# Performance work log

Hardware: AMD Instinct MI355X
Metric: run time of the kernel (lower is better)

Reference implementation:

```python
import jax, jax.numpy as jnp
import numpy as np

H, I, E, TOPK = 2048, 1408, 8, 2
B, S = 2, 2048


def setup_inputs() -> dict:
    key = jax.random.key(0)
    k1, k2, k3, k4, k5 = jax.random.split(key, 5)
    x = jax.random.normal(k1, (B, S, H), dtype=jnp.float32)
    expert_indices = jax.random.randint(k2, (B, S, TOPK), 0, E, dtype=jnp.int64)
    expert_weights = jax.random.uniform(k3, (B, S, TOPK), dtype=jnp.float32)
    # params: w13 = concat([gate, up], dim=1) -> [E, 2I, H]; down_proj [E, H, I]
    w13 = jax.random.normal(k4, (E, 2 * I, H), dtype=jnp.float32) * 0.02
    down_proj = jax.random.normal(k5, (E, H, I), dtype=jnp.float32) * 0.02
    return {"x": x, "expert_indices": expert_indices, "expert_weights": expert_weights,
            "w13": w13, "down_proj": down_proj}


def _moe(x, expert_indices, expert_weights, w13, down_proj):
    b, s, h = x.shape
    T = b * s
    x_flat = x.reshape(T, h)
    idx = expert_indices.reshape(T, -1)            # [T, top_k]
    wts = expert_weights.reshape(T, -1)            # [T, top_k]
    # dense combine weights: routing[t, e] = sum of weights of slots routed to e
    # (matches original scatter/index_add combine, including duplicate experts)
    routing = jnp.zeros((T, w13.shape[0]), x.dtype).at[
        jnp.arange(T)[:, None], idx].add(wts)      # [T, E]
    # per-expert SwiGLU MLP computed densely, zeroed out by routing weights
    gu = jnp.einsum('th,eih->tei', x_flat, w13)    # [T, E, 2I]
    g, u = jnp.split(gu, 2, axis=-1)
    hact = jax.nn.silu(g) * u                      # [T, E, I]
    y = jnp.einsum('tei,ehi->teh', hact, down_proj)  # [T, E, H]
    out = jnp.einsum('te,teh->th', routing, y)     # [T, H]
    return out.reshape(b, s, h)


def reference(x, expert_indices, expert_weights, w13, down_proj):
    return _moe(x, expert_indices, expert_weights, w13, down_proj)
```

## Files before the change

### kernel.cpp

```cpp
#include <hip/hip_runtime.h>
#include <hip/hip_bf16.h>


typedef __bf16 bf16;
typedef bf16 bf16x8 __attribute__((ext_vector_type(8)));
typedef float f32x4 __attribute__((ext_vector_type(4)));

constexpr int Hdim = 2048;
constexpr int Idim = 1408;
constexpr int NE = 8;
constexpr int TOPK = 2;
constexpr int NT = 4096;
constexpr int NPAIR = 8192;
constexpr int BK = 64;

#define GLOAD16(G, L) __builtin_amdgcn_global_load_lds(                    \
    (const __attribute__((address_space(1))) void*)(G),                    \
    (__attribute__((address_space(3))) void*)(L), 16, 0, 0)


__global__ void k_cvt(const float* __restrict__ src, bf16* __restrict__ dst, int n8) {
    int i = blockIdx.x * 256 + threadIdx.x;
    if (i >= n8) return;
    f32x4 a = *reinterpret_cast<const f32x4*>(src + (size_t)i * 8);
    f32x4 b = *reinterpret_cast<const f32x4*>(src + (size_t)i * 8 + 4);
    bf16x8 v;
#pragma unroll
    for (int j = 0; j < 4; j++) { v[j] = (bf16)a[j]; v[4 + j] = (bf16)b[j]; }
    *reinterpret_cast<bf16x8*>(dst + (size_t)i * 8) = v;
}


__global__ void k_bin1(const int* __restrict__ eidx, int* __restrict__ chunkhist) {
    __shared__ int h[NE];
    int t = threadIdx.x;
    if (t < NE) h[t] = 0;
    __syncthreads();
    int p = blockIdx.x * 256 + t;
    atomicAdd(&h[eidx[p]], 1);
    __syncthreads();
    if (t < NE) chunkhist[blockIdx.x * NE + t] = h[t];
}

__global__ void k_bin2(int* __restrict__ meta, const int* __restrict__ chunkhist,
                       int* __restrict__ chunkbase) {
    if (threadIdx.x == 0) {
        int counts[NE];
        for (int e = 0; e < NE; e++) counts[e] = 0;
        for (int b = 0; b < 32; b++)
            for (int e = 0; e < NE; e++) {
                chunkbase[b * NE + e] = counts[e];
                counts[e] += chunkhist[b * NE + e];
            }
        int acc = 0;
        for (int e = 0; e < NE; e++) {
            meta[e] = counts[e];
            meta[8 + e] = acc;
            acc += counts[e];
        }
    }
}

__global__ void k_bin3(const int* __restrict__ eidx, const float* __restrict__ wts,
                       const int* __restrict__ meta, const int* __restrict__ chunkbase,
                       int* __restrict__ token_id, float* __restrict__ weightv) {
    __shared__ int earr[256];
    int t = threadIdx.x;
    int p = blockIdx.x * 256 + t;
    int e = eidx[p];
    earr[t] = e;
    __syncthreads();
    int rank = 0;
    for (int q = 0; q < t; q++) rank += (earr[q] == e) ? 1 : 0;
    int pos = meta[8 + e] + chunkbase[blockIdx.x * NE + e] + rank;
    token_id[pos] = p / TOPK;
    weightv[pos] = wts[p];
}


__global__ __launch_bounds__(256, 2) void k_gemm1(
    const bf16* __restrict__ xb, const bf16* __restrict__ w13b,
    const int* __restrict__ meta, bf16* __restrict__ hact) {
    const int flat = blockIdx.x;
    const int work = (flat & 7) * 704 + (flat >> 3);
    const int mslot = work & 63;
    const int grp = work >> 6;
    const int e = grp / 11;
    const int ytile = grp - e * 11;

    const int n_e = meta[e];
    const int m0 = mslot * 128;
    if (m0 >= n_e) return;
    const int base = meta[8 + e];
    const int* toks = (const int*)(meta + 64) + base;
    const bf16* wg = w13b + (size_t)e * (2 * Idim) * Hdim + (size_t)(ytile * 128) * Hdim;
    const bf16* wu = wg + (size_t)Idim * Hdim;

    __shared__ bf16 As[128 * 64];
    __shared__ bf16 Bg[128 * 64];
    __shared__ bf16 Bu[128 * 64];

    const int tid = threadIdx.x;
    const int lane = tid & 63;
    const int wid = tid >> 6;
    const int wr = wid >> 1, wc = wid & 1;
    const int l16 = lane & 15, lq = lane >> 4;

    const bf16* gA[4];
    const bf16* gG[4];
    const bf16* gU[4];
    int lo[4];
#pragma unroll
    for (int r = 0; r < 4; r++) {
        int sid = r * 256 + tid;
        int row = sid >> 3, seg = sid & 7;
        int ss = seg ^ (row & 7);
        lo[r] = (r * 256 + (tid & ~63)) * 16;
        int rr = m0 + row;
        if (rr >= n_e) rr = n_e - 1;
        gA[r] = xb + (size_t)toks[rr] * Hdim + ss * 8;
        gG[r] = wg + (size_t)row * Hdim + ss * 8;
        gU[r] = wu + (size_t)row * Hdim + ss * 8;
    }

    f32x4 accg[4][4], accu[4][4];
#pragma unroll
    for (int m = 0; m < 4; m++)
#pragma unroll
        for (int n = 0; n < 4; n++) {
            accg[m][n] = f32x4{0.f, 0.f, 0.f, 0.f};
            accu[m][n] = f32x4{0.f, 0.f, 0.f, 0.f};
        }

    for (int k0 = 0; k0 < Hdim; k0 += BK) {
        __syncthreads();
#pragma unroll
        for (int r = 0; r < 4; r++) {
            GLOAD16(gA[r] + k0, (char*)As + lo[r]);
            GLOAD16(gG[r] + k0, (char*)Bg + lo[r]);
            GLOAD16(gU[r] + k0, (char*)Bu + lo[r]);
        }
        __syncthreads();
#pragma unroll
        for (int kk = 0; kk < 2; ++kk) {
            bf16x8 af[4], bgf[4], buf_[4];
#pragma unroll
            for (int m = 0; m < 4; m++) {
                int row = wr * 64 + m * 16 + l16;
                int s = (kk * 4 + lq) ^ (row & 7);
                af[m] = *reinterpret_cast<const bf16x8*>(&As[row * 64 + s * 8]);
            }
#pragma unroll
            for (int n = 0; n < 4; n++) {
                int row = wc * 64 + n * 16 + l16;
                int s = (kk * 4 + lq) ^ (row & 7);
                bgf[n] = *reinterpret_cast<const bf16x8*>(&Bg[row * 64 + s * 8]);
                buf_[n] = *reinterpret_cast<const bf16x8*>(&Bu[row * 64 + s * 8]);
            }
#pragma unroll
            for (int m = 0; m < 4; m++)
#pragma unroll
                for (int n = 0; n < 4; n++) {
                    accg[m][n] = __builtin_amdgcn_mfma_f32_16x16x32_bf16(af[m], bgf[n], accg[m][n], 0, 0, 0);
                    accu[m][n] = __builtin_amdgcn_mfma_f32_16x16x32_bf16(af[m], buf_[n], accu[m][n], 0, 0, 0);
                }
        }
    }

    const int colbase = ytile * 128 + wc * 64;
#pragma unroll
    for (int m = 0; m < 4; m++) {
        int lr0 = m0 + wr * 64 + m * 16 + lq * 4;
#pragma unroll
        for (int j = 0; j < 4; j++) {
            int lr = lr0 + j;
            if (lr < n_e) {
                size_t rowoff = (size_t)(base + lr) * Idim;
#pragma unroll
                for (int n = 0; n < 4; n++) {
                    float g = accg[m][n][j], u = accu[m][n][j];
                    float v = (g / (1.f + __expf(-g))) * u;
                    hact[rowoff + colbase + n * 16 + l16] = (bf16)v;
                }
            }
        }
    }
}


__global__ __launch_bounds__(256, 2) void k_gemm2(
    const bf16* __restrict__ hact, const bf16* __restrict__ dpb,
    const int* __restrict__ meta, const float* __restrict__ weightv,
    float* __restrict__ out) {
    const int flat = blockIdx.x;
    const int work = (flat & 7) * 1024 + (flat >> 3);
    const int mslot = work & 63;
    const int grp = work >> 6;
    const int e = grp >> 4;
    const int ytile = grp & 15;

    const int n_e = meta[e];
    const int m0 = mslot * 128;
    if (m0 >= n_e) return;
    const int base = meta[8 + e];
    const int* toks = (const int*)(meta + 64) + base;
    const bf16* wb = dpb + (size_t)e * Hdim * Idim + (size_t)(ytile * 128) * Idim;

    __shared__ bf16 As[128 * 64];
    __shared__ bf16 Bs[128 * 64];

    const int tid = threadIdx.x;
    const int lane = tid & 63;
    const int wid = tid >> 6;
    const int wr = wid >> 1, wc = wid & 1;
    const int l16 = lane & 15, lq = lane >> 4;

    const bf16* gA[4];
    const bf16* gB[4];
    int lo[4];
#pragma unroll
    for (int r = 0; r < 4; r++) {
        int sid = r * 256 + tid;
        int row = sid >> 3, seg = sid & 7;
        int ss = seg ^ (row & 7);
        lo[r] = (r * 256 + (tid & ~63)) * 16;
        int rr = m0 + row;
        if (rr >= n_e) rr = n_e - 1;
        gA[r] = hact + (size_t)(base + rr) * Idim + ss * 8;
        gB[r] = wb + (size_t)row * Idim + ss * 8;
    }

    f32x4 acc[4][4];
#pragma unroll
    for (int m = 0; m < 4; m++)
#pragma unroll
        for (int n = 0; n < 4; n++) acc[m][n] = f32x4{0.f, 0.f, 0.f, 0.f};

    for (int k0 = 0; k0 < Idim; k0 += BK) {
        __syncthreads();
#pragma unroll
        for (int r = 0; r < 4; r++) {
            GLOAD16(gA[r] + k0, (char*)As + lo[r]);
            GLOAD16(gB[r] + k0, (char*)Bs + lo[r]);
        }
        __syncthreads();
#pragma unroll
        for (int kk = 0; kk < 2; ++kk) {
            bf16x8 af[4], bf_[4];
#pragma unroll
            for (int m = 0; m < 4; m++) {
                int row = wr * 64 + m * 16 + l16;
                int s = (kk * 4 + lq) ^ (row & 7);
                af[m] = *reinterpret_cast<const bf16x8*>(&As[row * 64 + s * 8]);
            }
#pragma unroll
            for (int n = 0; n < 4; n++) {
                int row = wc * 64 + n * 16 + l16;
                int s = (kk * 4 + lq) ^ (row & 7);
                bf_[n] = *reinterpret_cast<const bf16x8*>(&Bs[row * 64 + s * 8]);
            }
#pragma unroll
            for (int m = 0; m < 4; m++)
#pragma unroll
                for (int n = 0; n < 4; n++)
                    acc[m][n] = __builtin_amdgcn_mfma_f32_16x16x32_bf16(af[m], bf_[n], acc[m][n], 0, 0, 0);
        }
    }

    const int colbase = ytile * 128 + wc * 64;
#pragma unroll
    for (int m = 0; m < 4; m++) {
        int lr0 = m0 + wr * 64 + m * 16 + lq * 4;
#pragma unroll
        for (int j = 0; j < 4; j++) {
            int lr = lr0 + j;
            if (lr < n_e) {
                int tok = toks[lr];
                float w = weightv[base + lr];
#pragma unroll
                for (int n = 0; n < 4; n++) {
                    float v = acc[m][n][j] * w;
                    unsafeAtomicAdd(&out[(size_t)tok * Hdim + colbase + n * 16 + l16], v);
                }
            }
        }
    }
}


extern "C" void kernel_launch(void* const* d_in, const int* in_sizes, int n_in,
                              void* d_out, int out_size, void* d_ws, size_t ws_size,
                              hipStream_t stream) {
    const float* x = (const float*)d_in[0];
    const int* eidx = (const int*)d_in[1];
    const float* ewts = (const float*)d_in[2];
    const float* w13 = (const float*)d_in[3];
    const float* dproj = (const float*)d_in[4];
    float* out = (float*)d_out;

    char* ws = (char*)d_ws;
    int* meta = (int*)ws;
    int* token_id = meta + 64;
    float* weightv = (float*)(meta + 64 + NPAIR);
    int* chunkhist = meta + 64 + 2 * NPAIR;
    int* chunkbase = chunkhist + 256;
    bf16* xb = (bf16*)(ws + 67840);
    bf16* w13b = xb + (size_t)NT * Hdim;
    bf16* dpb = w13b + (size_t)NE * 2 * Idim * Hdim;
    bf16* hact = dpb + (size_t)NE * Hdim * Idim;

    hipMemsetAsync(d_out, 0, (size_t)out_size * sizeof(float), stream);

    const int nx8 = NT * Hdim / 8;
    const int nw8 = NE * 2 * Idim * Hdim / 8;
    const int nd8 = NE * Hdim * Idim / 8;
    k_cvt<<<(nx8 + 255) / 256, 256, 0, stream>>>(x, xb, nx8);
    k_cvt<<<(nw8 + 255) / 256, 256, 0, stream>>>(w13, w13b, nw8);
    k_cvt<<<(nd8 + 255) / 256, 256, 0, stream>>>(dproj, dpb, nd8);

    k_bin1<<<32, 256, 0, stream>>>(eidx, chunkhist);
    k_bin2<<<1, 64, 0, stream>>>(meta, chunkhist, chunkbase);
    k_bin3<<<32, 256, 0, stream>>>(eidx, ewts, meta, chunkbase, token_id, weightv);

    k_gemm1<<<5632, 256, 0, stream>>>(xb, w13b, meta, hact);
    k_gemm2<<<8192, 256, 0, stream>>>(hact, dpb, meta, weightv, out);
}
```

Before: 354.5 us.

## Double-buffer LDS with BK=32 stages in both MoE GEMM kernels

```diff
diff --git a/kernel.cpp b/kernel.cpp
--- a/kernel.cpp
+++ b/kernel.cpp
@@ -12,7 +12,6 @@
 constexpr int TOPK = 2;
 constexpr int NT = 4096;
 constexpr int NPAIR = 8192;
-constexpr int BK = 64;
 
 #define GLOAD16(G, L) __builtin_amdgcn_global_load_lds(                    \
     (const __attribute__((address_space(1))) void*)(G),                    \
@@ -78,7 +77,7 @@
 }
 
 
-__global__ __launch_bounds__(256, 2) void k_gemm1(
+__global__ __launch_bounds__(256, 3) void k_gemm1(
     const bf16* __restrict__ xb, const bf16* __restrict__ w13b,
     const int* __restrict__ meta, bf16* __restrict__ hact) {
     const int flat = blockIdx.x;
@@ -96,9 +95,8 @@
     const bf16* wg = w13b + (size_t)e * (2 * Idim) * Hdim + (size_t)(ytile * 128) * Hdim;
     const bf16* wu = wg + (size_t)Idim * Hdim;
 
-    __shared__ bf16 As[128 * 64];
-    __shared__ bf16 Bg[128 * 64];
-    __shared__ bf16 Bu[128 * 64];
+    __shared__ bf16 buf0[12288];
+    __shared__ bf16 buf1[12288];
 
     const int tid = threadIdx.x;
     const int lane = tid & 63;
@@ -106,21 +104,24 @@
     const int wr = wid >> 1, wc = wid & 1;
     const int l16 = lane & 15, lq = lane >> 4;
 
-    const bf16* gA[4];
-    const bf16* gG[4];
-    const bf16* gU[4];
-    int lo[4];
-#pragma unroll
-    for (int r = 0; r < 4; r++) {
-        int sid = r * 256 + tid;
-        int row = sid >> 3, seg = sid & 7;
-        int ss = seg ^ (row & 7);
-        lo[r] = (r * 256 + (tid & ~63)) * 16;
-        int rr = m0 + row;
-        if (rr >= n_e) rr = n_e - 1;
-        gA[r] = xb + (size_t)toks[rr] * Hdim + ss * 8;
-        gG[r] = wg + (size_t)row * Hdim + ss * 8;
-        gU[r] = wu + (size_t)row * Hdim + ss * 8;
+    const bf16* gp[6];
+    int lo[6];
+#pragma unroll
+    for (int r = 0; r < 6; r++) {
+        int rr = r & 1;
+        int s = rr * 256 + tid;
+        int row = s >> 2, seg = s & 3;
+        int ss = seg ^ ((row >> 1) & 3);
+        lo[r] = (r >> 1) * 8192 + (rr * 256 + (tid & ~63)) * 16;
+        if (r < 2) {
+            int rm = m0 + row;
+            if (rm >= n_e) rm = n_e - 1;
+            gp[r] = xb + (size_t)toks[rm] * Hdim + ss * 8;
+        } else if (r < 4) {
+            gp[r] = wg + (size_t)row * Hdim + ss * 8;
+        } else {
+            gp[r] = wu + (size_t)row * Hdim + ss * 8;
+        }
     }
 
     f32x4 accg[4][4], accu[4][4];
@@ -132,39 +133,49 @@
             accu[m][n] = f32x4{0.f, 0.f, 0.f, 0.f};
         }
 
-    for (int k0 = 0; k0 < Hdim; k0 += BK) {
+#define STAGE1(BUF, K0)                                                     \
+    {                                                                       \
+        _Pragma("unroll")                                                   \
+        for (int r = 0; r < 6; r++) GLOAD16(gp[r] + (K0), (char*)(BUF) + lo[r]); \
+    }
+
+#define COMP1(BUF)                                                          \
+    {                                                                       \
+        const bf16* As_ = (BUF);                                            \
+        const bf16* Bg_ = (BUF) + 4096;                                     \
+        const bf16* Bu_ = (BUF) + 8192;                                     \
+        bf16x8 af[4], bgf[4], buf_[4];                                      \
+        _Pragma("unroll")                                                   \
+        for (int m = 0; m < 4; m++) {                                       \
+            int row = wr * 64 + m * 16 + l16;                               \
+            int s = lq ^ ((row >> 1) & 3);                                  \
+            af[m] = *reinterpret_cast<const bf16x8*>(&As_[row * 32 + s * 8]); \
+        }                                                                   \
+        _Pragma("unroll")                                                   \
+        for (int n = 0; n < 4; n++) {                                       \
+            int row = wc * 64 + n * 16 + l16;                               \
+            int s = lq ^ ((row >> 1) & 3);                                  \
+            bgf[n] = *reinterpret_cast<const bf16x8*>(&Bg_[row * 32 + s * 8]); \
+            buf_[n] = *reinterpret_cast<const bf16x8*>(&Bu_[row * 32 + s * 8]); \
+        }                                                                   \
+        _Pragma("unroll")                                                   \
+        for (int m = 0; m < 4; m++)                                         \
+            _Pragma("unroll")                                               \
+            for (int n = 0; n < 4; n++) {                                   \
+                accg[m][n] = __builtin_amdgcn_mfma_f32_16x16x32_bf16(af[m], bgf[n], accg[m][n], 0, 0, 0); \
+                accu[m][n] = __builtin_amdgcn_mfma_f32_16x16x32_bf16(af[m], buf_[n], accu[m][n], 0, 0, 0); \
+            }                                                               \
+    }
+
+    STAGE1(buf0, 0);
+    __syncthreads();
+    for (int k = 0; k < Hdim; k += 64) {
+        STAGE1(buf1, k + 32);
+        COMP1(buf0);
         __syncthreads();
-#pragma unroll
-        for (int r = 0; r < 4; r++) {
-            GLOAD16(gA[r] + k0, (char*)As + lo[r]);
-            GLOAD16(gG[r] + k0, (char*)Bg + lo[r]);
-            GLOAD16(gU[r] + k0, (char*)Bu + lo[r]);
-        }
+        if (k + 64 < Hdim) STAGE1(buf0, k + 64);
+        COMP1(buf1);
         __syncthreads();
-#pragma unroll
-        for (int kk = 0; kk < 2; ++kk) {
-            bf16x8 af[4], bgf[4], buf_[4];
-#pragma unroll
-            for (int m = 0; m < 4; m++) {
-                int row = wr * 64 + m * 16 + l16;
-                int s = (kk * 4 + lq) ^ (row & 7);
-                af[m] = *reinterpret_cast<const bf16x8*>(&As[row * 64 + s * 8]);
-            }
-#pragma unroll
-            for (int n = 0; n < 4; n++) {
-                int row = wc * 64 + n * 16 + l16;
-                int s = (kk * 4 + lq) ^ (row & 7);
-                bgf[n] = *reinterpret_cast<const bf16x8*>(&Bg[row * 64 + s * 8]);
-                buf_[n] = *reinterpret_cast<const bf16x8*>(&Bu[row * 64 + s * 8]);
-            }
-#pragma unroll
-            for (int m = 0; m < 4; m++)
-#pragma unroll
-                for (int n = 0; n < 4; n++) {
-                    accg[m][n] = __builtin_amdgcn_mfma_f32_16x16x32_bf16(af[m], bgf[n], accg[m][n], 0, 0, 0);
-                    accu[m][n] = __builtin_amdgcn_mfma_f32_16x16x32_bf16(af[m], buf_[n], accu[m][n], 0, 0, 0);
-                }
-        }
     }
 
     const int colbase = ytile * 128 + wc * 64;
@@ -185,10 +196,12 @@
             }
         }
     }
-}
-
-
-__global__ __launch_bounds__(256, 2) void k_gemm2(
+#undef STAGE1
+#undef COMP1
+}
+
+
+__global__ __launch_bounds__(256, 4) void k_gemm2(
     const bf16* __restrict__ hact, const bf16* __restrict__ dpb,
     const int* __restrict__ meta, const float* __restrict__ weightv,
     float* __restrict__ out) {
@@ -206,8 +219,8 @@
     const int* toks = (const int*)(meta + 64) + base;
     const bf16* wb = dpb + (size_t)e * Hdim * Idim + (size_t)(ytile * 128) * Idim;
 
-    __shared__ bf16 As[128 * 64];
-    __shared__ bf16 Bs[128 * 64];
+    __shared__ bf16 c0[8192];
+    __shared__ bf16 c1[8192];
 
     const int tid = threadIdx.x;
     const int lane = tid & 63;
@@ -215,19 +228,22 @@
     const int wr = wid >> 1, wc = wid & 1;
     const int l16 = lane & 15, lq = lane >> 4;
 
-    const bf16* gA[4];
-    const bf16* gB[4];
+    const bf16* gp[4];
     int lo[4];
 #pragma unroll
     for (int r = 0; r < 4; r++) {
-        int sid = r * 256 + tid;
-        int row = sid >> 3, seg = sid & 7;
-        int ss = seg ^ (row & 7);
-        lo[r] = (r * 256 + (tid & ~63)) * 16;
-        int rr = m0 + row;
-        if (rr >= n_e) rr = n_e - 1;
-        gA[r] = hact + (size_t)(base + rr) * Idim + ss * 8;
-        gB[r] = wb + (size_t)row * Idim + ss * 8;
+        int rr = r & 1;
+        int s = rr * 256 + tid;
+        int row = s >> 2, seg = s & 3;
+        int ss = seg ^ ((row >> 1) & 3);
+        lo[r] = (r >> 1) * 8192 + (rr * 256 + (tid & ~63)) * 16;
+        if (r < 2) {
+            int rm = m0 + row;
+            if (rm >= n_e) rm = n_e - 1;
+            gp[r] = hact + (size_t)(base + rm) * Idim + ss * 8;
+        } else {
+            gp[r] = wb + (size_t)row * Idim + ss * 8;
+        }
     }
 
     f32x4 acc[4][4];
@@ -236,35 +252,45 @@
 #pragma unroll
         for (int n = 0; n < 4; n++) acc[m][n] = f32x4{0.f, 0.f, 0.f, 0.f};
 
-    for (int k0 = 0; k0 < Idim; k0 += BK) {
+#define STAGE2(BUF, K0)                                                     \
+    {                                                                       \
+        _Pragma("unroll")                                                   \
+        for (int r = 0; r < 4; r++) GLOAD16(gp[r] + (K0), (char*)(BUF) + lo[r]); \
+    }
+
+#define COMP2(BUF)                                                          \
+    {                                                                       \
+        const bf16* As_ = (BUF);                                            \
+        const bf16* Bs_ = (BUF) + 4096;                                     \
+        bf16x8 af[4], bf_[4];                                               \
+        _Pragma("unroll")                                                   \
+        for (int m = 0; m < 4; m++) {                                       \
+            int row = wr * 64 + m * 16 + l16;                               \
+            int s = lq ^ ((row >> 1) & 3);                                  \
+            af[m] = *reinterpret_cast<const bf16x8*>(&As_[row * 32 + s * 8]); \
+        }                                                                   \
+        _Pragma("unroll")                                                   \
+        for (int n = 0; n < 4; n++) {                                       \
+            int row = wc * 64 + n * 16 + l16;                               \
+            int s = lq ^ ((row >> 1) & 3);                                  \
+            bf_[n] = *reinterpret_cast<const bf16x8*>(&Bs_[row * 32 + s * 8]); \
+        }                                                                   \
+        _Pragma("unroll")                                                   \
+        for (int m = 0; m < 4; m++)                                         \
+            _Pragma("unroll")                                               \
+            for (int n = 0; n < 4; n++)                                     \
+                acc[m][n] = __builtin_amdgcn_mfma_f32_16x16x32_bf16(af[m], bf_[n], acc[m][n], 0, 0, 0); \
+    }
+
+    STAGE2(c0, 0);
+    __syncthreads();
+    for (int k = 0; k < Idim; k += 64) {
+        STAGE2(c1, k + 32);
+        COMP2(c0);
         __syncthreads();
-#pragma unroll
-        for (int r = 0; r < 4; r++) {
-            GLOAD16(gA[r] + k0, (char*)As + lo[r]);
-            GLOAD16(gB[r] + k0, (char*)Bs + lo[r]);
-        }
+        if (k + 64 < Idim) STAGE2(c0, k + 64);
+        COMP2(c1);
         __syncthreads();
-#pragma unroll
-        for (int kk = 0; kk < 2; ++kk) {
-            bf16x8 af[4], bf_[4];
-#pragma unroll
-            for (int m = 0; m < 4; m++) {
-                int row = wr * 64 + m * 16 + l16;
-                int s = (kk * 4 + lq) ^ (row & 7);
-                af[m] = *reinterpret_cast<const bf16x8*>(&As[row * 64 + s * 8]);
-            }
-#pragma unroll
-            for (int n = 0; n < 4; n++) {
-                int row = wc * 64 + n * 16 + l16;
-                int s = (kk * 4 + lq) ^ (row & 7);
-                bf_[n] = *reinterpret_cast<const bf16x8*>(&Bs[row * 64 + s * 8]);
-            }
-#pragma unroll
-            for (int m = 0; m < 4; m++)
-#pragma unroll
-                for (int n = 0; n < 4; n++)
-                    acc[m][n] = __builtin_amdgcn_mfma_f32_16x16x32_bf16(af[m], bf_[n], acc[m][n], 0, 0, 0);
-        }
     }
 
     const int colbase = ytile * 128 + wc * 64;
@@ -285,6 +311,8 @@
             }
         }
     }
+#undef STAGE2
+#undef COMP2
 }
 
 
```

Result: slower. 802.4 us (+126.3%).

## Enlarge M tile to 256 rows in both grouped MoE GEMMs

Applied to the files above, without the earlier changes.

```diff
diff --git a/kernel.cpp b/kernel.cpp
--- a/kernel.cpp
+++ b/kernel.cpp
@@ -78,27 +78,137 @@
 }
 
 
-__global__ __launch_bounds__(256, 2) void k_gemm1(
+__global__ __launch_bounds__(512, 2) void k_gemm1(
     const bf16* __restrict__ xb, const bf16* __restrict__ w13b,
     const int* __restrict__ meta, bf16* __restrict__ hact) {
     const int flat = blockIdx.x;
-    const int work = (flat & 7) * 704 + (flat >> 3);
-    const int mslot = work & 63;
-    const int grp = work >> 6;
+    const int work = (flat & 7) * 352 + (flat >> 3);
+    const int mslot = work & 31;
+    const int grp = work >> 5;
     const int e = grp / 11;
     const int ytile = grp - e * 11;
 
     const int n_e = meta[e];
-    const int m0 = mslot * 128;
+    const int m0 = mslot * 256;
     if (m0 >= n_e) return;
     const int base = meta[8 + e];
     const int* toks = (const int*)(meta + 64) + base;
     const bf16* wg = w13b + (size_t)e * (2 * Idim) * Hdim + (size_t)(ytile * 128) * Hdim;
     const bf16* wu = wg + (size_t)Idim * Hdim;
 
-    __shared__ bf16 As[128 * 64];
-    __shared__ bf16 Bg[128 * 64];
-    __shared__ bf16 Bu[128 * 64];
+    __shared__ bf16 smem[32768];
+
+    const int tid = threadIdx.x;
+    const int lane = tid & 63;
+    const int wid = tid >> 6;
+    const int wr = wid >> 2, wc = wid & 3;
+    const int l16 = lane & 15, lq = lane >> 4;
+
+    const bf16* gp[8];
+    int lo[8];
+#pragma unroll
+    for (int r = 0; r < 8; r++) {
+        int q = (r < 4) ? r : ((r - 4) & 1);
+        int sid = q * 512 + tid;
+        int row = sid >> 3, seg = sid & 7;
+        int ss = seg ^ (row & 7);
+        if (r < 4) {
+            lo[r] = (r * 512 + (tid & ~63)) * 16;
+            int rm = m0 + row;
+            if (rm >= n_e) rm = n_e - 1;
+            gp[r] = xb + (size_t)toks[rm] * Hdim + ss * 8;
+        } else if (r < 6) {
+            lo[r] = 32768 + ((r - 4) * 512 + (tid & ~63)) * 16;
+            gp[r] = wg + (size_t)row * Hdim + ss * 8;
+        } else {
+            lo[r] = 49152 + ((r - 6) * 512 + (tid & ~63)) * 16;
+            gp[r] = wu + (size_t)row * Hdim + ss * 8;
+        }
+    }
+
+    f32x4 accg[8][2], accu[8][2];
+#pragma unroll
+    for (int m = 0; m < 8; m++)
+#pragma unroll
+        for (int n = 0; n < 2; n++) {
+            accg[m][n] = f32x4{0.f, 0.f, 0.f, 0.f};
+            accu[m][n] = f32x4{0.f, 0.f, 0.f, 0.f};
+        }
+
+    for (int k0 = 0; k0 < Hdim; k0 += BK) {
+        __syncthreads();
+#pragma unroll
+        for (int r = 0; r < 8; r++) GLOAD16(gp[r] + k0, (char*)smem + lo[r]);
+        __syncthreads();
+        const bf16* As = smem;
+        const bf16* Bg = smem + 16384;
+        const bf16* Bu = smem + 24576;
+#pragma unroll
+        for (int kk = 0; kk < 2; ++kk) {
+            bf16x8 af[8], bgf[2], buf_[2];
+#pragma unroll
+            for (int m = 0; m < 8; m++) {
+                int row = wr * 128 + m * 16 + l16;
+                int s = (kk * 4 + lq) ^ (row & 7);
+                af[m] = *reinterpret_cast<const bf16x8*>(&As[row * 64 + s * 8]);
+            }
+#pragma unroll
+            for (int n = 0; n < 2; n++) {
+                int row = wc * 32 + n * 16 + l16;
+                int s = (kk * 4 + lq) ^ (row & 7);
+                bgf[n] = *reinterpret_cast<const bf16x8*>(&Bg[row * 64 + s * 8]);
+                buf_[n] = *reinterpret_cast<const bf16x8*>(&Bu[row * 64 + s * 8]);
+            }
+#pragma unroll
+            for (int m = 0; m < 8; m++)
+#pragma unroll
+                for (int n = 0; n < 2; n++) {
+                    accg[m][n] = __builtin_amdgcn_mfma_f32_16x16x32_bf16(af[m], bgf[n], accg[m][n], 0, 0, 0);
+                    accu[m][n] = __builtin_amdgcn_mfma_f32_16x16x32_bf16(af[m], buf_[n], accu[m][n], 0, 0, 0);
+                }
+        }
+    }
+
+    const int colbase = ytile * 128 + wc * 32;
+#pragma unroll
+    for (int m = 0; m < 8; m++) {
+        int lr0 = m0 + wr * 128 + m * 16 + lq * 4;
+#pragma unroll
+        for (int j = 0; j < 4; j++) {
+            int lr = lr0 + j;
+            if (lr < n_e) {
+                size_t rowoff = (size_t)(base + lr) * Idim;
+#pragma unroll
+                for (int n = 0; n < 2; n++) {
+                    float g = accg[m][n][j], u = accu[m][n][j];
+                    float v = (g / (1.f + __expf(-g))) * u;
+                    hact[rowoff + colbase + n * 16 + l16] = (bf16)v;
+                }
+            }
+        }
+    }
+}
+
+
+__global__ __launch_bounds__(256, 3) void k_gemm2(
+    const bf16* __restrict__ hact, const bf16* __restrict__ dpb,
+    const int* __restrict__ meta, const float* __restrict__ weightv,
+    float* __restrict__ out) {
+    const int flat = blockIdx.x;
+    const int work = (flat & 7) * 512 + (flat >> 3);
+    const int mslot = work & 31;
+    const int grp = work >> 5;
+    const int e = grp >> 4;
+    const int ytile = grp & 15;
+
+    const int n_e = meta[e];
+    const int m0 = mslot * 256;
+    if (m0 >= n_e) return;
+    const int base = meta[8 + e];
+    const int* toks = (const int*)(meta + 64) + base;
+    const bf16* wb = dpb + (size_t)e * Hdim * Idim + (size_t)(ytile * 128) * Idim;
+
+    __shared__ bf16 smem[24576];
 
     const int tid = threadIdx.x;
     const int lane = tid & 63;
@@ -106,150 +216,44 @@
     const int wr = wid >> 1, wc = wid & 1;
     const int l16 = lane & 15, lq = lane >> 4;
 
-    const bf16* gA[4];
-    const bf16* gG[4];
-    const bf16* gU[4];
-    int lo[4];
-#pragma unroll
-    for (int r = 0; r < 4; r++) {
-        int sid = r * 256 + tid;
+    const bf16* gp[12];
+    int lo[12];
+#pragma unroll
+    for (int r = 0; r < 12; r++) {
+        int q = (r < 8) ? r : (r - 8);
+        int sid = q * 256 + tid;
         int row = sid >> 3, seg = sid & 7;
         int ss = seg ^ (row & 7);
-        lo[r] = (r * 256 + (tid & ~63)) * 16;
-        int rr = m0 + row;
-        if (rr >= n_e) rr = n_e - 1;
-        gA[r] = xb + (size_t)toks[rr] * Hdim + ss * 8;
-        gG[r] = wg + (size_t)row * Hdim + ss * 8;
-        gU[r] = wu + (size_t)row * Hdim + ss * 8;
-    }
-
-    f32x4 accg[4][4], accu[4][4];
-#pragma unroll
-    for (int m = 0; m < 4; m++)
-#pragma unroll
-        for (int n = 0; n < 4; n++) {
-            accg[m][n] = f32x4{0.f, 0.f, 0.f, 0.f};
-            accu[m][n] = f32x4{0.f, 0.f, 0.f, 0.f};
-        }
-
-    for (int k0 = 0; k0 < Hdim; k0 += BK) {
-        __syncthreads();
-#pragma unroll
-        for (int r = 0; r < 4; r++) {
-            GLOAD16(gA[r] + k0, (char*)As + lo[r]);
-            GLOAD16(gG[r] + k0, (char*)Bg + lo[r]);
-            GLOAD16(gU[r] + k0, (char*)Bu + lo[r]);
-        }
-        __syncthreads();
-#pragma unroll
-        for (int kk = 0; kk < 2; ++kk) {
-            bf16x8 af[4], bgf[4], buf_[4];
-#pragma unroll
-            for (int m = 0; m < 4; m++) {
-                int row = wr * 64 + m * 16 + l16;
-                int s = (kk * 4 + lq) ^ (row & 7);
-                af[m] = *reinterpret_cast<const bf16x8*>(&As[row * 64 + s * 8]);
-            }
-#pragma unroll
-            for (int n = 0; n < 4; n++) {
-                int row = wc * 64 + n * 16 + l16;
-                int s = (kk * 4 + lq) ^ (row & 7);
-                bgf[n] = *reinterpret_cast<const bf16x8*>(&Bg[row * 64 + s * 8]);
-                buf_[n] = *reinterpret_cast<const bf16x8*>(&Bu[row * 64 + s * 8]);
-            }
-#pragma unroll
-            for (int m = 0; m < 4; m++)
-#pragma unroll
-                for (int n = 0; n < 4; n++) {
-                    accg[m][n] = __builtin_amdgcn_mfma_f32_16x16x32_bf16(af[m], bgf[n], accg[m][n], 0, 0, 0);
-                    accu[m][n] = __builtin_amdgcn_mfma_f32_16x16x32_bf16(af[m], buf_[n], accu[m][n], 0, 0, 0);
-                }
-        }
-    }
-
-    const int colbase = ytile * 128 + wc * 64;
-#pragma unroll
-    for (int m = 0; m < 4; m++) {
-        int lr0 = m0 + wr * 64 + m * 16 + lq * 4;
-#pragma unroll
-        for (int j = 0; j < 4; j++) {
-            int lr = lr0 + j;
-            if (lr < n_e) {
-                size_t rowoff = (size_t)(base + lr) * Idim;
-#pragma unroll
-                for (int n = 0; n < 4; n++) {
-                    float g = accg[m][n][j], u = accu[m][n][j];
-                    float v = (g / (1.f + __expf(-g))) * u;
-                    hact[rowoff + colbase + n * 16 + l16] = (bf16)v;
-                }
-            }
-        }
-    }
-}
-
-
-__global__ __launch_bounds__(256, 2) void k_gemm2(
-    const bf16* __restrict__ hact, const bf16* __restrict__ dpb,
-    const int* __restrict__ meta, const float* __restrict__ weightv,
-    float* __restrict__ out) {
-    const int flat = blockIdx.x;
-    const int work = (flat & 7) * 1024 + (flat >> 3);
-    const int mslot = work & 63;
-    const int grp = work >> 6;
-    const int e = grp >> 4;
-    const int ytile = grp & 15;
-
-    const int n_e = meta[e];
-    const int m0 = mslot * 128;
-    if (m0 >= n_e) return;
-    const int base = meta[8 + e];
-    const int* toks = (const int*)(meta + 64) + base;
-    const bf16* wb = dpb + (size_t)e * Hdim * Idim + (size_t)(ytile * 128) * Idim;
-
-    __shared__ bf16 As[128 * 64];
-    __shared__ bf16 Bs[128 * 64];
-
-    const int tid = threadIdx.x;
-    const int lane = tid & 63;
-    const int wid = tid >> 6;
-    const int wr = wid >> 1, wc = wid & 1;
-    const int l16 = lane & 15, lq = lane >> 4;
-
-    const bf16* gA[4];
-    const bf16* gB[4];
-    int lo[4];
-#pragma unroll
-    for (int r = 0; r < 4; r++) {
-        int sid = r * 256 + tid;
-        int row = sid >> 3, seg = sid & 7;
-        int ss = seg ^ (row & 7);
-        lo[r] = (r * 256 + (tid & ~63)) * 16;
-        int rr = m0 + row;
-        if (rr >= n_e) rr = n_e - 1;
-        gA[r] = hact + (size_t)(base + rr) * Idim + ss * 8;
-        gB[r] = wb + (size_t)row * Idim + ss * 8;
-    }
-
-    f32x4 acc[4][4];
-#pragma unroll
-    for (int m = 0; m < 4; m++)
+        if (r < 8) {
+            lo[r] = (r * 256 + (tid & ~63)) * 16;
+            int rm = m0 + row;
+            if (rm >= n_e) rm = n_e - 1;
+            gp[r] = hact + (size_t)(base + rm) * Idim + ss * 8;
+        } else {
+            lo[r] = 32768 + ((r - 8) * 256 + (tid & ~63)) * 16;
+            gp[r] = wb + (size_t)row * Idim + ss * 8;
+        }
+    }
+
+    f32x4 acc[8][4];
+#pragma unroll
+    for (int m = 0; m < 8; m++)
 #pragma unroll
         for (int n = 0; n < 4; n++) acc[m][n] = f32x4{0.f, 0.f, 0.f, 0.f};
 
     for (int k0 = 0; k0 < Idim; k0 += BK) {
         __syncthreads();
 #pragma unroll
-        for (int r = 0; r < 4; r++) {
-            GLOAD16(gA[r] + k0, (char*)As + lo[r]);
-            GLOAD16(gB[r] + k0, (char*)Bs + lo[r]);
-        }
+        for (int r = 0; r < 12; r++) GLOAD16(gp[r] + k0, (char*)smem + lo[r]);
         __syncthreads();
+        const bf16* As = smem;
+        const bf16* Bs = smem + 16384;
 #pragma unroll
         for (int kk = 0; kk < 2; ++kk) {
-            bf16x8 af[4], bf_[4];
-#pragma unroll
-            for (int m = 0; m < 4; m++) {
-                int row = wr * 64 + m * 16 + l16;
+            bf16x8 af[8], bf_[4];
+#pragma unroll
+            for (int m = 0; m < 8; m++) {
+                int row = wr * 128 + m * 16 + l16;
                 int s = (kk * 4 + lq) ^ (row & 7);
                 af[m] = *reinterpret_cast<const bf16x8*>(&As[row * 64 + s * 8]);
             }
@@ -260,7 +264,7 @@
                 bf_[n] = *reinterpret_cast<const bf16x8*>(&Bs[row * 64 + s * 8]);
             }
 #pragma unroll
-            for (int m = 0; m < 4; m++)
+            for (int m = 0; m < 8; m++)
 #pragma unroll
                 for (int n = 0; n < 4; n++)
                     acc[m][n] = __builtin_amdgcn_mfma_f32_16x16x32_bf16(af[m], bf_[n], acc[m][n], 0, 0, 0);
@@ -269,8 +273,8 @@
 
     const int colbase = ytile * 128 + wc * 64;
 #pragma unroll
-    for (int m = 0; m < 4; m++) {
-        int lr0 = m0 + wr * 64 + m * 16 + lq * 4;
+    for (int m = 0; m < 8; m++) {
+        int lr0 = m0 + wr * 128 + m * 16 + lq * 4;
 #pragma unroll
         for (int j = 0; j < 4; j++) {
             int lr = lr0 + j;
@@ -322,6 +326,6 @@
     k_bin2<<<1, 64, 0, stream>>>(meta, chunkhist, chunkbase);
     k_bin3<<<32, 256, 0, stream>>>(eidx, ewts, meta, chunkbase, token_id, weightv);
 
-    k_gemm1<<<5632, 256, 0, stream>>>(xb, w13b, meta, hact);
-    k_gemm2<<<8192, 256, 0, stream>>>(hact, dpb, meta, weightv, out);
-}
+    k_gemm1<<<2816, 512, 0, stream>>>(xb, w13b, meta, hact);
+    k_gemm2<<<4096, 256, 0, stream>>>(hact, dpb, meta, weightv, out);
+}
```

Result: slower. 510.3 us (+43.9%).
